# Kernel tuning notes

Hardware: AMD Instinct MI355X
Metric: run time of the kernel (lower is better)

Reference implementation:

```python
import jax, jax.numpy as jnp
import numpy as np

D_MODEL = 256      # num_nodes == d_model (forced by pre_relation mask shape)
MW = 2             # moving_window (hardcoded '2' in MPNN reshape)
STRIDE = 1
DECAY = 0.7
INPUT_DIM = 64
OUTPUT_DIM = 64
BN_EPS = 1e-5


def _mask_matrix():
    # Mask_Matrix: block (i,j) of size d_model x d_model equals decay**|i-j|
    blocks = DECAY ** np.abs(np.arange(MW)[:, None] - np.arange(MW)[None, :])
    return jnp.asarray(np.kron(blocks, np.ones((D_MODEL, D_MODEL))).astype(np.float32))


def _bn(h, w, b):
    # training-mode BatchNorm1d over channel-last layout [B, N, C]
    mu = h.mean(axis=(0, 1))
    var = h.var(axis=(0, 1))  # biased variance, as torch uses for normalization
    return (h - mu) * jax.lax.rsqrt(var + BN_EPS) * w + b


def setup_inputs() -> dict:
    key = jax.random.key(0)
    ks = jax.random.split(key, 4)
    bs, scale_num = 16, 17
    x = jax.random.normal(ks[0], (bs, scale_num, D_MODEL, INPUT_DIM), jnp.float32)
    # mapping2 weights scaled small to keep the dot-product softmax well conditioned
    w_map2 = jax.random.normal(ks[1], (INPUT_DIM, INPUT_DIM), jnp.float32) * 0.05
    b_map2 = jnp.zeros((INPUT_DIM,), jnp.float32)
    bn0_w = jnp.ones((INPUT_DIM,), jnp.float32)
    bn0_b = jnp.zeros((INPUT_DIM,), jnp.float32)
    th0_w = jax.random.normal(ks[2], (OUTPUT_DIM, INPUT_DIM), jnp.float32) / np.float32(np.sqrt(INPUT_DIM))
    th0_b = jnp.zeros((OUTPUT_DIM,), jnp.float32)
    th1_w = jax.random.normal(ks[3], (OUTPUT_DIM, INPUT_DIM), jnp.float32) / np.float32(np.sqrt(INPUT_DIM))
    th1_b = jnp.zeros((OUTPUT_DIM,), jnp.float32)
    bn1_w = jnp.ones((OUTPUT_DIM,), jnp.float32)
    bn1_b = jnp.zeros((OUTPUT_DIM,), jnp.float32)
    return dict(x=x, w_map2=w_map2, b_map2=b_map2, bn0_w=bn0_w, bn0_b=bn0_b,
                th0_w=th0_w, th0_b=th0_b, th1_w=th1_w, th1_b=th1_b,
                bn1_w=bn1_w, bn1_b=bn1_b)


def reference(x, w_map2, b_map2, bn0_w, bn0_b, th0_w, th0_b, th1_w, th1_b, bn1_w, bn1_b):
    bs, S, N, F = x.shape
    L = (S - MW) // STRIDE + 1  # num_windows from F.unfold
    # WindowConv_Graph + transpose(2,3) + reshape: X[b,l,m,n,f] = x[b, l*stride+m, n, f]
    idx = np.arange(L)[:, None] * STRIDE + np.arange(MW)[None, :]
    X = x[:, idx].reshape(bs * L, MW * N, F)  # [B', N1, F]

    # Dot_Graph_Construction_weights (N1 != d_model -> mapping2 branch)
    nf = X @ w_map2.T + b_map2                       # [B', N1, F]
    adj = jnp.einsum('bnf,bmf->bnm', nf, nf)         # [B', N1, N1]
    eye = jnp.eye(MW * N, dtype=x.dtype)
    adj = jax.nn.leaky_relu(adj - eye * 1e8)
    adj = jax.nn.softmax(adj, axis=-1) + eye

    # decay mask multiply
    adj = adj * _mask_matrix()

    # BatchNorm over input_dim channels
    xb = _bn(nf, bn0_w, bn0_b)

    # MPNN_mk_v2, field=2, way='sum'
    out = (adj @ xb) @ th0_w.T + th0_b               # hop 1
    adj2 = adj @ adj
    out = out + (adj2 @ xb) @ th1_w.T + th1_b        # hop 2
    out = jax.nn.leaky_relu(_bn(out, bn1_w, bn1_b))

    # pooling over the moving_window axis (mean), then over windows (mean)
    out = out.reshape(bs, L, MW, N, OUTPUT_DIM).mean(axis=2)
    return out.mean(axis=1)  # [bs, num_nodes, output_dim]
```

## Files before the change

### kernel.cpp

```cpp
#include <hip/hip_runtime.h>


typedef unsigned short u16;
typedef __bf16 bf16x8 __attribute__((ext_vector_type(8)));
typedef float f32x4 __attribute__((ext_vector_type(4)));
typedef unsigned int u32x4 __attribute__((ext_vector_type(4)));

#define MFMA16(a, b, c) __builtin_amdgcn_mfma_f32_16x16x32_bf16(a, b, c, 0, 0, 0)

#define BSZ 16
#define SNUM 17
#define FD 64
#define NB 256
#define N1 512
#define SL_ELEMS 16384
#define Y_ELEMS (BSZ * SNUM * SL_ELEMS)

#define WM_O 0
#define BM_O 4096
#define B0W_O 4160
#define B0B_O 4224
#define T0W_O 4288
#define T0B_O 8384
#define T1W_O 8448
#define T1B_O 12544
#define B1W_O 12608
#define B1B_O 12672
#define P_TOT 12736

#define SLAB2_O 32768
#define RED_O 65536
#define SCR_O 65792
#define LDS_U16 (SCR_O + 16 * 640)

__device__ __forceinline__ float bf2f(u16 u) {
    union { unsigned int i; float f; } v;
    v.i = ((unsigned int)u) << 16;
    return v.f;
}
__device__ __forceinline__ u16 f2bu(float f) {
    __bf16 h = (__bf16)f;
    return __builtin_bit_cast(u16, h);
}
__device__ __forceinline__ u16 f2bf(float f) {
    unsigned int u = __builtin_bit_cast(unsigned int, f);
    unsigned int r = (u + 0x7fffu + ((u >> 16) & 1u)) >> 16;
    return (u16)r;
}
__device__ __forceinline__ bf16x8 ld8g(const u16* p) {
    return __builtin_bit_cast(bf16x8, *reinterpret_cast<const u32x4*>(p));
}

__global__ __launch_bounds__(256) void k_prep(
    const void* p0, const void* p1, const void* p2, const void* p3,
    const void* p4, const void* p5, const void* p6, const void* p7,
    const void* p8, const void* p9, int* __restrict__ flagOut,
    u16* __restrict__ pc, float* __restrict__ stats) {
    const int tid = threadIdx.x, lane = tid & 63;
    int z = 0, bc = 0;
    const unsigned int* w = (const unsigned int*)p0;
    for (int i = lane; i < 2048; i += 64) {
        const unsigned int v = w[i];
        z += ((v & 0xffffu) == 0u);
        bc += (v >> 14) & 1;
    }
#pragma unroll
    for (int o = 1; o < 64; o <<= 1) {
        z += __shfl_xor(z, o);
        bc += __shfl_xor(bc, o);
    }
    const int flag = (z > 1024 || bc > 256) ? 1 : 0;
    if (blockIdx.x == 0) {
        if (tid == 0) *flagOut = flag;
        if (tid < 256) stats[tid] = 0.f;
    }
    const int i = blockIdx.x * 256 + tid;
    if (i >= P_TOT) return;
    const void* src;
    int si;
    if (i < BM_O)        { src = p0; si = i; }
    else if (i < B0W_O)  { src = p1; si = i - BM_O; }
    else if (i < B0B_O)  { src = p2; si = i - B0W_O; }
    else if (i < T0W_O)  { src = p3; si = i - B0B_O; }
    else if (i < T0B_O)  { src = p4; si = i - T0W_O; }
    else if (i < T1W_O)  { src = p5; si = i - T0B_O; }
    else if (i < T1B_O)  { src = p6; si = i - T1W_O; }
    else if (i < B1W_O)  { src = p7; si = i - T1B_O; }
    else if (i < B1B_O)  { src = p8; si = i - B1W_O; }
    else                 { src = p9; si = i - B1B_O; }
    pc[i] = flag ? f2bf(((const float*)src)[si]) : ((const u16*)src)[si];
}

__global__ __launch_bounds__(256) void k_y(const void* __restrict__ xv,
                                           const int* __restrict__ flag,
                                           const u16* __restrict__ pc,
                                           u16* __restrict__ y,
                                           float* __restrict__ gstats) {
    const int slice = blockIdx.x;
    const int tid = threadIdx.x, wave = tid >> 6, lane = tid & 63;
    const int quad = lane >> 4, l16 = lane & 15;
    __shared__ float red[128];
    if (tid < 128) red[tid] = 0.f;
    const int isf32 = *flag;

    f32x4 acc[4][4];
#pragma unroll
    for (int i = 0; i < 4; i++)
#pragma unroll
        for (int j = 0; j < 4; j++) acc[i][j] = (f32x4){0.f, 0.f, 0.f, 0.f};

    bf16x8 bfr[4][2];
#pragma unroll
    for (int nt = 0; nt < 4; nt++)
#pragma unroll
        for (int kh = 0; kh < 2; kh++)
            bfr[nt][kh] = ld8g(pc + WM_O + (nt * 16 + l16) * 64 + kh * 32 + quad * 8);

    const float* xf = (const float*)xv + (size_t)slice * SL_ELEMS;
    const u16* xh = (const u16*)xv + (size_t)slice * SL_ELEMS;

#pragma unroll
    for (int mt = 0; mt < 4; mt++) {
        const int row = wave * 64 + mt * 16 + l16;
        bf16x8 a0, a1;
        if (isf32) {
            const float* r0 = xf + row * 64 + quad * 8;
            f32x4 v0 = *(const f32x4*)r0;
            f32x4 v1 = *(const f32x4*)(r0 + 4);
            f32x4 v2 = *(const f32x4*)(r0 + 32);
            f32x4 v3 = *(const f32x4*)(r0 + 36);
#pragma unroll
            for (int j = 0; j < 4; j++) {
                a0[j] = (__bf16)v0[j]; a0[4 + j] = (__bf16)v1[j];
                a1[j] = (__bf16)v2[j]; a1[4 + j] = (__bf16)v3[j];
            }
        } else {
            a0 = ld8g(xh + row * 64 + quad * 8);
            a1 = ld8g(xh + row * 64 + 32 + quad * 8);
        }
#pragma unroll
        for (int nt = 0; nt < 4; nt++)
            acc[mt][nt] = MFMA16(a1, bfr[nt][1], MFMA16(a0, bfr[nt][0], acc[mt][nt]));
    }

    u16* ys = y + (size_t)slice * SL_ELEMS;
    float s1[4] = {0.f, 0.f, 0.f, 0.f}, s2[4] = {0.f, 0.f, 0.f, 0.f};
#pragma unroll
    for (int nt = 0; nt < 4; nt++) {
        const int col = nt * 16 + l16;
        const float bias = bf2f(pc[BM_O + col]);
#pragma unroll
        for (int mt = 0; mt < 4; mt++)
#pragma unroll
            for (int r = 0; r < 4; r++) {
                const int row = wave * 64 + mt * 16 + quad * 4 + r;
                const float v = acc[mt][nt][r] + bias;
                ys[row * 64 + col] = f2bu(v);
                s1[nt] += v;
                s2[nt] += v * v;
            }
        s1[nt] += __shfl_xor(s1[nt], 16); s1[nt] += __shfl_xor(s1[nt], 32);
        s2[nt] += __shfl_xor(s2[nt], 16); s2[nt] += __shfl_xor(s2[nt], 32);
    }
    __syncthreads();
    if (quad == 0) {
#pragma unroll
        for (int nt = 0; nt < 4; nt++) {
            atomicAdd(&red[nt * 16 + l16], s1[nt]);
            atomicAdd(&red[64 + nt * 16 + l16], s2[nt]);
        }
    }
    __syncthreads();
    const int s = slice % SNUM;
    const float wgt = (s == 0 || s == SNUM - 1) ? 1.f : 2.f;
    if (tid < 128) atomicAdd(&gstats[tid], red[tid] * wgt);
}

__global__ __launch_bounds__(1024)
__attribute__((amdgpu_waves_per_eu(4, 4)))
void k_mega(
    const u16* __restrict__ y, float* __restrict__ stats,
    const u16* __restrict__ pc, u16* __restrict__ opre) {
    __shared__ u16 lds[LDS_U16];
    u16* slab1 = lds;
    u16* slab2 = lds + SLAB2_O;
    float* red = (float*)(lds + RED_O);
    const int tid = threadIdx.x, w = tid >> 6, lane = tid & 63;
    const int quad = lane >> 4, l16 = lane & 15;
    u16* scr = lds + SCR_O + w * 640;
    const int p = blockIdx.x, b = p >> 4, l = p & 15;
    const f32x4 ZERO4 = (f32x4){0.f, 0.f, 0.f, 0.f};

    if (tid < 128) red[tid] = 0.f;

    const float cinv = 1.f / 131072.f;
    const int fme = tid & 63;
    float mu0 = stats[fme] * cinv;
    float vr0 = fmaxf(stats[64 + fme] * cinv - mu0 * mu0, 0.f);
    const float scale_f = rsqrtf(vr0 + 1e-5f) * bf2f(pc[B0W_O + fme]);
    const float shift_f = bf2f(pc[B0B_O + fme]) - mu0 * scale_f;

    const u16* ybase = y + (size_t)(b * SNUM + l) * SL_ELEMS;
#pragma unroll
    for (int i = 0; i < 4; i++) {
        const int gid = i * 1024 + tid, n = gid >> 3, g = gid & 7;
        *(u32x4*)(slab1 + n * 64 + ((g ^ (n & 7)) << 3)) =
            *(const u32x4*)(ybase + n * 64 + g * 8);
    }
    __syncthreads();

#pragma unroll
    for (int i = 0; i < 4; i++) {
        const int gn = (tid >> 6) + i * 16;
        union { u16 u[8]; u32x4 v; } pk;
#pragma unroll
        for (int j = 0; j < 8; j++) {
            const int n = gn * 8 + j;
            const u16 raw = slab1[n * 64 + (((fme >> 3) ^ (n & 7)) << 3) + (fme & 7)];
            pk.u[j] = f2bu(bf2f(raw) * scale_f + shift_f);
        }
        *(u32x4*)(slab2 + fme * 512 + ((gn ^ fme) << 3)) = pk.v;
    }
    __syncthreads();

    bf16x8 a[2][2];
#pragma unroll
    for (int st = 0; st < 2; st++)
#pragma unroll
        for (int h = 0; h < 2; h++) {
            const int row = w * 32 + st * 16 + l16;
            a[st][h] = *(const bf16x8*)(slab1 + row * 64 + (((h * 4 + quad) ^ (row & 7)) << 3));
        }

    const float mb = (w < 8) ? 0.7f : (1.0f / 0.7f);
    const float me = (w < 8) ? (1.0f / 0.7f) : 1.0f;

#pragma unroll 1
    for (int pass = 0; pass < 2; pass++) {
        f32x4 oacc[2][4];
        f32x4 lsum[2];
#pragma unroll
        for (int st = 0; st < 2; st++) {
            lsum[st] = ZERO4;
#pragma unroll
            for (int ft = 0; ft < 4; ft++) oacc[st][ft] = ZERO4;
        }

#pragma unroll 1
        for (int c = 0; c < 8; c++) {
            if (c == 4) {
#pragma unroll
                for (int st = 0; st < 2; st++)
#pragma unroll
                    for (int r = 0; r < 4; r++) lsum[st][r] *= mb;
            }
            const float lmf = ((w >= 8) == (c >= 4)) ? 0.f : -0.5145731728f;
#pragma unroll
            for (int ch = 0; ch < 2; ch++) {
                const int colbase = c * 64 + ch * 32;
                f32x4 S[2][2];
#pragma unroll
                for (int jt = 0; jt < 2; jt++) {
                    const int rj = colbase + jt * 16 + l16;
                    const bf16x8 b0 = *(const bf16x8*)(slab1 + rj * 64 + ((quad ^ (rj & 7)) << 3));
                    const bf16x8 b1 = *(const bf16x8*)(slab1 + rj * 64 + (((4 + quad) ^ (rj & 7)) << 3));
#pragma unroll
                    for (int st = 0; st < 2; st++)
                        S[st][jt] = MFMA16(a[st][1], b1, MFMA16(a[st][0], b0, ZERO4));
                }
                bf16x8 pa[2];
#pragma unroll
                for (int st = 0; st < 2; st++) {
                    const int rowbase = w * 32 + st * 16;
#pragma unroll
                    for (int jt = 0; jt < 2; jt++)
#pragma unroll
                        for (int r = 0; r < 4; r++) {
                            const float s = S[st][jt][r];
                            const float m2 = s > 0.f ? 1.44269504f : 0.0144269504f;
                            float pv = exp2f(fminf(fmaf(s, m2, lmf), 86.f));
                            if (colbase + jt * 16 == rowbase && l16 == quad * 4 + r) pv = 0.f;
                            lsum[st][r] += pv;
                            scr[(quad * 4 + r) * 40 + jt * 16 + l16] = f2bu(pv);
                        }
                    pa[st] = *(const bf16x8*)(scr + l16 * 40 + quad * 8);
                }
#pragma unroll
                for (int ft = 0; ft < 4; ft++) {
                    const int f = ft * 16 + l16, gn = c * 8 + ch * 4 + quad;
                    const bf16x8 bv = *(const bf16x8*)(slab2 + f * 512 + ((gn ^ f) << 3));
                    oacc[0][ft] = MFMA16(pa[0], bv, oacc[0][ft]);
                    oacc[1][ft] = MFMA16(pa[1], bv, oacc[1][ft]);
                }
            }
        }
#pragma unroll
        for (int st = 0; st < 2; st++)
#pragma unroll
            for (int r = 0; r < 4; r++) {
                lsum[st][r] += __shfl_xor(lsum[st][r], 1);
                lsum[st][r] += __shfl_xor(lsum[st][r], 2);
                lsum[st][r] += __shfl_xor(lsum[st][r], 4);
                lsum[st][r] += __shfl_xor(lsum[st][r], 8);
            }

        if (pass == 0) {
#pragma unroll
            for (int st = 0; st < 2; st++) {
                f32x4 inv;
#pragma unroll
                for (int r = 0; r < 4; r++) inv[r] = __builtin_amdgcn_rcpf(lsum[st][r] * me);
#pragma unroll
                for (int ft = 0; ft < 4; ft++)
#pragma unroll
                    for (int r = 0; r < 4; r++) {
                        const int i = w * 32 + st * 16 + quad * 4 + r;
                        const int f = ft * 16 + l16;
                        const float xbv = bf2f(slab2[f * 512 + (((i >> 3) ^ f) << 3) + (i & 7)]);
                        oacc[st][ft][r] = oacc[st][ft][r] * inv[r] + xbv;
                    }
            }
            __syncthreads();
#pragma unroll
            for (int st = 0; st < 2; st++)
#pragma unroll
                for (int ft = 0; ft < 4; ft++)
#pragma unroll
                    for (int r = 0; r < 4; r++) {
                        const int i = w * 32 + st * 16 + quad * 4 + r;
                        const int f = ft * 16 + l16;
                        slab2[f * 512 + (((i >> 3) ^ f) << 3) + (i & 7)] = f2bu(oacc[st][ft][r]);
                    }
            __syncthreads();
        } else {
            float s1a[4] = {0.f, 0.f, 0.f, 0.f}, s2a[4] = {0.f, 0.f, 0.f, 0.f};
#pragma unroll
            for (int st = 0; st < 2; st++) {
                f32x4 inv;
#pragma unroll
                for (int r = 0; r < 4; r++) inv[r] = __builtin_amdgcn_rcpf(lsum[st][r] * me);
#pragma unroll
                for (int ft = 0; ft < 4; ft++)
#pragma unroll
                    for (int r = 0; r < 4; r++) {
                        const int i = w * 32 + st * 16 + quad * 4 + r;
                        const int f = ft * 16 + l16;
                        const float o1 = bf2f(slab2[f * 512 + (((i >> 3) ^ f) << 3) + (i & 7)]);
                        oacc[st][ft][r] = oacc[st][ft][r] * inv[r] + o1;
                    }
                bf16x8 a1[2], a2[2];
                const int irow = w * 32 + st * 16 + l16;
#pragma unroll
                for (int h = 0; h < 2; h++)
#pragma unroll
                    for (int j = 0; j < 8; j++) {
                        const int f = h * 32 + quad * 8 + j;
                        const u16 raw = slab2[f * 512 + (((irow >> 3) ^ f) << 3) + (irow & 7)];
                        a1[h][j] = __builtin_bit_cast(__bf16, raw);
                    }
#pragma unroll
                for (int h = 0; h < 2; h++) {
#pragma unroll
                    for (int ftl = 0; ftl < 2; ftl++)
#pragma unroll
                        for (int r = 0; r < 4; r++)
                            scr[(quad * 4 + r) * 40 + ftl * 16 + l16] = f2bu(oacc[st][2 * h + ftl][r]);
                    a2[h] = *(const bf16x8*)(scr + l16 * 40 + quad * 8);
                }
                f32x4 pacc[4];
#pragma unroll
                for (int ot = 0; ot < 4; ot++) {
                    const int o = ot * 16 + l16;
                    const float bias = bf2f(pc[T0B_O + o]) + bf2f(pc[T1B_O + o]);
                    pacc[ot] = (f32x4){bias, bias, bias, bias};
                }
#pragma unroll
                for (int h = 0; h < 2; h++)
#pragma unroll
                    for (int ot = 0; ot < 4; ot++) {
                        const int o = ot * 16 + l16;
                        bf16x8 w0f = ld8g(pc + T0W_O + o * 64 + h * 32 + quad * 8);
                        bf16x8 w1f = ld8g(pc + T1W_O + o * 64 + h * 32 + quad * 8);
                        pacc[ot] = MFMA16(a1[h], w0f, pacc[ot]);
                        pacc[ot] = MFMA16(a2[h], w1f, pacc[ot]);
                    }
#pragma unroll
                for (int ot = 0; ot < 4; ot++)
#pragma unroll
                    for (int r = 0; r < 4; r++) {
                        const int i = w * 32 + st * 16 + quad * 4 + r;
                        const int o = ot * 16 + l16;
                        const float v = pacc[ot][r];
                        s1a[ot] += v;
                        s2a[ot] += v * v;
                        opre[(size_t)p * (N1 * FD) + (size_t)i * 64 + o] = f2bu(v);
                    }
            }
#pragma unroll
            for (int ot = 0; ot < 4; ot++) {
                s1a[ot] += __shfl_xor(s1a[ot], 16); s1a[ot] += __shfl_xor(s1a[ot], 32);
                s2a[ot] += __shfl_xor(s2a[ot], 16); s2a[ot] += __shfl_xor(s2a[ot], 32);
            }
            if (quad == 0) {
#pragma unroll
                for (int ot = 0; ot < 4; ot++) {
                    atomicAdd(&red[ot * 16 + l16], s1a[ot]);
                    atomicAdd(&red[64 + ot * 16 + l16], s2a[ot]);
                }
            }
            __syncthreads();
            if (tid < 128) atomicAdd(&stats[128 + tid], red[tid]);
        }
    }
}

__global__ __launch_bounds__(256) void k_final(const u16* __restrict__ op,
                                               const float* __restrict__ stats,
                                               const u16* __restrict__ pc,
                                               float* __restrict__ out) {
    const int o = blockIdx.x * 256 + threadIdx.x;
    const int f = o & 63, n = (o >> 6) & 255, b = o >> 14;
    const float inv = 1.f / 131072.f;
    const float mu = stats[128 + f] * inv;
    const float var = fmaxf(stats[192 + f] * inv - mu * mu, 0.f);
    const float rs = rsqrtf(var + 1e-5f);
    const float scale = rs * bf2f(pc[B1W_O + f]);
    const float shift = bf2f(pc[B1B_O + f]) - mu * scale;
    float acc = 0.f;
    for (int l = 0; l < 16; l++) {
        const size_t pb = (size_t)(b * 16 + l) * N1 * FD;
#pragma unroll
        for (int m = 0; m < 2; m++) {
            float v = bf2f(op[pb + (size_t)(m * 256 + n) * 64 + f]);
            v = v * scale + shift;
            acc += (v > 0.f ? v : 0.01f * v);
        }
    }
    out[o] = acc * (1.f / 32.f);
}

extern "C" void kernel_launch(void* const* d_in, const int* in_sizes, int n_in,
                              void* d_out, int out_size, void* d_ws, size_t ws_size,
                              hipStream_t stream) {
    char* ws = (char*)d_ws;
    size_t off = 0;
    auto alloc = [&](size_t bytes) { void* pp = ws + off; off += (bytes + 255) & ~(size_t)255; return pp; };
    u16* y = (u16*)alloc((size_t)Y_ELEMS * 2);
    u16* opre = (u16*)alloc((size_t)NB * N1 * FD * 2);
    u16* pc = (u16*)alloc(P_TOT * 2);
    float* stats = (float*)alloc(256 * 4);
    int* flag = (int*)alloc(256);
    float* out = (float*)d_out;

    k_prep<<<50, 256, 0, stream>>>(d_in[1], d_in[2], d_in[3], d_in[4], d_in[5],
                                   d_in[6], d_in[7], d_in[8], d_in[9], d_in[10],
                                   flag, pc, stats);
    k_y<<<BSZ * SNUM, 256, 0, stream>>>(d_in[0], flag, pc, y, stats);
    k_mega<<<NB, 1024, 0, stream>>>(y, stats, pc, opre);
    k_final<<<1024, 256, 0, stream>>>(opre, stats, pc, out);
}
```

Before: 200.8 us.

## Split mega kernel into two hop kernels over half-row blocks

```diff
diff --git a/kernel.cpp b/kernel.cpp
--- a/kernel.cpp
+++ b/kernel.cpp
@@ -31,7 +31,7 @@
 #define SLAB2_O 32768
 #define RED_O 65536
 #define SCR_O 65792
-#define LDS_U16 (SCR_O + 16 * 640)
+#define LDS_U16 (SCR_O + 8 * 640)
 
 __device__ __forceinline__ float bf2f(u16 u) {
     union { unsigned int i; float f; } v;
@@ -176,11 +176,157 @@
     if (tid < 128) atomicAdd(&gstats[tid], red[tid] * wgt);
 }
 
-__global__ __launch_bounds__(1024)
-__attribute__((amdgpu_waves_per_eu(4, 4)))
-void k_mega(
-    const u16* __restrict__ y, float* __restrict__ stats,
-    const u16* __restrict__ pc, u16* __restrict__ opre) {
+__device__ __forceinline__ void stage_slab1(u16* slab1, const u16* ybase,
+                                            int tid) {
+#pragma unroll
+    for (int i = 0; i < 8; i++) {
+        const int gid = i * 512 + tid, n = gid >> 3, g = gid & 7;
+        *(u32x4*)(slab1 + n * 64 + ((g ^ (n & 7)) << 3)) =
+            *(const u32x4*)(ybase + n * 64 + g * 8);
+    }
+}
+
+__global__ __launch_bounds__(512)
+__attribute__((amdgpu_waves_per_eu(2, 2)))
+void k_h1(const u16* __restrict__ y, const float* __restrict__ stats,
+          const u16* __restrict__ pc, u16* __restrict__ z1g) {
+    __shared__ u16 lds[LDS_U16];
+    u16* slab1 = lds;
+    u16* slab2 = lds + SLAB2_O;
+    const int tid = threadIdx.x, w = tid >> 6, lane = tid & 63;
+    const int quad = lane >> 4, l16 = lane & 15;
+    u16* scr = lds + SCR_O + w * 640;
+    const int g = blockIdx.x, p = g >> 1, half = g & 1;
+    const int b = p >> 4, l = p & 15;
+    const f32x4 ZERO4 = (f32x4){0.f, 0.f, 0.f, 0.f};
+
+    const float cinv = 1.f / 131072.f;
+    const int fme = tid & 63;
+    float mu0 = stats[fme] * cinv;
+    float vr0 = fmaxf(stats[64 + fme] * cinv - mu0 * mu0, 0.f);
+    const float scale_f = rsqrtf(vr0 + 1e-5f) * bf2f(pc[B0W_O + fme]);
+    const float shift_f = bf2f(pc[B0B_O + fme]) - mu0 * scale_f;
+
+    const u16* ybase = y + (size_t)(b * SNUM + l) * SL_ELEMS;
+    stage_slab1(slab1, ybase, tid);
+    __syncthreads();
+
+#pragma unroll
+    for (int i = 0; i < 8; i++) {
+        const int gn = w + i * 8;
+        union { u16 u[8]; u32x4 v; } pk;
+#pragma unroll
+        for (int j = 0; j < 8; j++) {
+            const int n = gn * 8 + j;
+            const u16 raw = slab1[n * 64 + (((fme >> 3) ^ (n & 7)) << 3) + (fme & 7)];
+            pk.u[j] = f2bu(bf2f(raw) * scale_f + shift_f);
+        }
+        *(u32x4*)(slab2 + fme * 512 + ((gn ^ fme) << 3)) = pk.v;
+    }
+    __syncthreads();
+
+    bf16x8 a[2][2];
+#pragma unroll
+    for (int st = 0; st < 2; st++)
+#pragma unroll
+        for (int h = 0; h < 2; h++) {
+            const int row = half * 256 + w * 32 + st * 16 + l16;
+            a[st][h] = *(const bf16x8*)(slab1 + row * 64 + (((h * 4 + quad) ^ (row & 7)) << 3));
+        }
+
+    const float mb = (half == 0) ? 0.7f : (1.0f / 0.7f);
+    const float me = (half == 0) ? (1.0f / 0.7f) : 1.0f;
+
+    f32x4 oacc[2][4];
+    f32x4 lsum[2];
+#pragma unroll
+    for (int st = 0; st < 2; st++) {
+        lsum[st] = ZERO4;
+#pragma unroll
+        for (int ft = 0; ft < 4; ft++) oacc[st][ft] = ZERO4;
+    }
+
+#pragma unroll 1
+    for (int c = 0; c < 8; c++) {
+        if (c == 4) {
+#pragma unroll
+            for (int st = 0; st < 2; st++)
+#pragma unroll
+                for (int r = 0; r < 4; r++) lsum[st][r] *= mb;
+        }
+        const float lmf = ((half == 1) == (c >= 4)) ? 0.f : -0.5145731728f;
+#pragma unroll
+        for (int ch = 0; ch < 2; ch++) {
+            const int colbase = c * 64 + ch * 32;
+            f32x4 S[2][2];
+#pragma unroll
+            for (int jt = 0; jt < 2; jt++) {
+                const int rj = colbase + jt * 16 + l16;
+                const bf16x8 b0 = *(const bf16x8*)(slab1 + rj * 64 + ((quad ^ (rj & 7)) << 3));
+                const bf16x8 b1 = *(const bf16x8*)(slab1 + rj * 64 + (((4 + quad) ^ (rj & 7)) << 3));
+#pragma unroll
+                for (int st = 0; st < 2; st++)
+                    S[st][jt] = MFMA16(a[st][1], b1, MFMA16(a[st][0], b0, ZERO4));
+            }
+            bf16x8 pa[2];
+#pragma unroll
+            for (int st = 0; st < 2; st++) {
+                const int rowbase = half * 256 + w * 32 + st * 16;
+#pragma unroll
+                for (int jt = 0; jt < 2; jt++)
+#pragma unroll
+                    for (int r = 0; r < 4; r++) {
+                        const float s = S[st][jt][r];
+                        const float m2 = s > 0.f ? 1.44269504f : 0.0144269504f;
+                        float pv = exp2f(fminf(fmaf(s, m2, lmf), 86.f));
+                        if (colbase + jt * 16 == rowbase && l16 == quad * 4 + r) pv = 0.f;
+                        lsum[st][r] += pv;
+                        scr[(quad * 4 + r) * 40 + jt * 16 + l16] = f2bu(pv);
+                    }
+                pa[st] = *(const bf16x8*)(scr + l16 * 40 + quad * 8);
+            }
+#pragma unroll
+            for (int ft = 0; ft < 4; ft++) {
+                const int f = ft * 16 + l16, gn = c * 8 + ch * 4 + quad;
+                const bf16x8 bv = *(const bf16x8*)(slab2 + f * 512 + ((gn ^ f) << 3));
+                oacc[0][ft] = MFMA16(pa[0], bv, oacc[0][ft]);
+                oacc[1][ft] = MFMA16(pa[1], bv, oacc[1][ft]);
+            }
+        }
+    }
+#pragma unroll
+    for (int st = 0; st < 2; st++)
+#pragma unroll
+        for (int r = 0; r < 4; r++) {
+            lsum[st][r] += __shfl_xor(lsum[st][r], 1);
+            lsum[st][r] += __shfl_xor(lsum[st][r], 2);
+            lsum[st][r] += __shfl_xor(lsum[st][r], 4);
+            lsum[st][r] += __shfl_xor(lsum[st][r], 8);
+        }
+
+#pragma unroll
+    for (int st = 0; st < 2; st++) {
+        f32x4 inv;
+#pragma unroll
+        for (int r = 0; r < 4; r++) inv[r] = __builtin_amdgcn_rcpf(lsum[st][r] * me);
+#pragma unroll
+        for (int ft = 0; ft < 4; ft++)
+#pragma unroll
+            for (int r = 0; r < 4; r++) {
+                const int i = half * 256 + w * 32 + st * 16 + quad * 4 + r;
+                const int f = ft * 16 + l16;
+                const float xbv = bf2f(slab2[f * 512 + (((i >> 3) ^ f) << 3) + (i & 7)]);
+                z1g[(size_t)p * (N1 * FD) + (size_t)i * 64 + f] =
+                    f2bu(oacc[st][ft][r] * inv[r] + xbv);
+            }
+    }
+}
+
+__global__ __launch_bounds__(512)
+__attribute__((amdgpu_waves_per_eu(2, 2)))
+void k_h2(const u16* __restrict__ y, const u16* __restrict__ z1g,
+          float* __restrict__ stats, const u16* __restrict__ pc,
+          u16* __restrict__ opre) {
     __shared__ u16 lds[LDS_U16];
     u16* slab1 = lds;
     u16* slab2 = lds + SLAB2_O;
@@ -188,36 +334,25 @@
     const int tid = threadIdx.x, w = tid >> 6, lane = tid & 63;
     const int quad = lane >> 4, l16 = lane & 15;
     u16* scr = lds + SCR_O + w * 640;
-    const int p = blockIdx.x, b = p >> 4, l = p & 15;
+    const int g = blockIdx.x, p = g >> 1, half = g & 1;
+    const int b = p >> 4, l = p & 15;
     const f32x4 ZERO4 = (f32x4){0.f, 0.f, 0.f, 0.f};
+    const int fme = tid & 63;
 
     if (tid < 128) red[tid] = 0.f;
 
-    const float cinv = 1.f / 131072.f;
-    const int fme = tid & 63;
-    float mu0 = stats[fme] * cinv;
-    float vr0 = fmaxf(stats[64 + fme] * cinv - mu0 * mu0, 0.f);
-    const float scale_f = rsqrtf(vr0 + 1e-5f) * bf2f(pc[B0W_O + fme]);
-    const float shift_f = bf2f(pc[B0B_O + fme]) - mu0 * scale_f;
-
     const u16* ybase = y + (size_t)(b * SNUM + l) * SL_ELEMS;
-#pragma unroll
-    for (int i = 0; i < 4; i++) {
-        const int gid = i * 1024 + tid, n = gid >> 3, g = gid & 7;
-        *(u32x4*)(slab1 + n * 64 + ((g ^ (n & 7)) << 3)) =
-            *(const u32x4*)(ybase + n * 64 + g * 8);
-    }
-    __syncthreads();
-
-#pragma unroll
-    for (int i = 0; i < 4; i++) {
-        const int gn = (tid >> 6) + i * 16;
+    stage_slab1(slab1, ybase, tid);
+
+    const u16* zbase = z1g + (size_t)p * (N1 * FD);
+#pragma unroll
+    for (int i = 0; i < 8; i++) {
+        const int gn = w + i * 8;
         union { u16 u[8]; u32x4 v; } pk;
 #pragma unroll
         for (int j = 0; j < 8; j++) {
             const int n = gn * 8 + j;
-            const u16 raw = slab1[n * 64 + (((fme >> 3) ^ (n & 7)) << 3) + (fme & 7)];
-            pk.u[j] = f2bu(bf2f(raw) * scale_f + shift_f);
+            pk.u[j] = zbase[n * 64 + fme];
         }
         *(u32x4*)(slab2 + fme * 512 + ((gn ^ fme) << 3)) = pk.v;
     }
@@ -228,190 +363,157 @@
     for (int st = 0; st < 2; st++)
 #pragma unroll
         for (int h = 0; h < 2; h++) {
-            const int row = w * 32 + st * 16 + l16;
+            const int row = half * 256 + w * 32 + st * 16 + l16;
             a[st][h] = *(const bf16x8*)(slab1 + row * 64 + (((h * 4 + quad) ^ (row & 7)) << 3));
         }
 
-    const float mb = (w < 8) ? 0.7f : (1.0f / 0.7f);
-    const float me = (w < 8) ? (1.0f / 0.7f) : 1.0f;
+    const float mb = (half == 0) ? 0.7f : (1.0f / 0.7f);
+    const float me = (half == 0) ? (1.0f / 0.7f) : 1.0f;
+
+    f32x4 oacc[2][4];
+    f32x4 lsum[2];
+#pragma unroll
+    for (int st = 0; st < 2; st++) {
+        lsum[st] = ZERO4;
+#pragma unroll
+        for (int ft = 0; ft < 4; ft++) oacc[st][ft] = ZERO4;
+    }
 
 #pragma unroll 1
-    for (int pass = 0; pass < 2; pass++) {
-        f32x4 oacc[2][4];
-        f32x4 lsum[2];
-#pragma unroll
-        for (int st = 0; st < 2; st++) {
-            lsum[st] = ZERO4;
-#pragma unroll
-            for (int ft = 0; ft < 4; ft++) oacc[st][ft] = ZERO4;
-        }
-
-#pragma unroll 1
-        for (int c = 0; c < 8; c++) {
-            if (c == 4) {
+    for (int c = 0; c < 8; c++) {
+        if (c == 4) {
+#pragma unroll
+            for (int st = 0; st < 2; st++)
+#pragma unroll
+                for (int r = 0; r < 4; r++) lsum[st][r] *= mb;
+        }
+        const float lmf = ((half == 1) == (c >= 4)) ? 0.f : -0.5145731728f;
+#pragma unroll
+        for (int ch = 0; ch < 2; ch++) {
+            const int colbase = c * 64 + ch * 32;
+            f32x4 S[2][2];
+#pragma unroll
+            for (int jt = 0; jt < 2; jt++) {
+                const int rj = colbase + jt * 16 + l16;
+                const bf16x8 b0 = *(const bf16x8*)(slab1 + rj * 64 + ((quad ^ (rj & 7)) << 3));
+                const bf16x8 b1 = *(const bf16x8*)(slab1 + rj * 64 + (((4 + quad) ^ (rj & 7)) << 3));
 #pragma unroll
                 for (int st = 0; st < 2; st++)
-#pragma unroll
-                    for (int r = 0; r < 4; r++) lsum[st][r] *= mb;
-            }
-            const float lmf = ((w >= 8) == (c >= 4)) ? 0.f : -0.5145731728f;
-#pragma unroll
-            for (int ch = 0; ch < 2; ch++) {
-                const int colbase = c * 64 + ch * 32;
-                f32x4 S[2][2];
-#pragma unroll
-                for (int jt = 0; jt < 2; jt++) {
-                    const int rj = colbase + jt * 16 + l16;
-                    const bf16x8 b0 = *(const bf16x8*)(slab1 + rj * 64 + ((quad ^ (rj & 7)) << 3));
-                    const bf16x8 b1 = *(const bf16x8*)(slab1 + rj * 64 + (((4 + quad) ^ (rj & 7)) << 3));
-#pragma unroll
-                    for (int st = 0; st < 2; st++)
-                        S[st][jt] = MFMA16(a[st][1], b1, MFMA16(a[st][0], b0, ZERO4));
-                }
-                bf16x8 pa[2];
-#pragma unroll
-                for (int st = 0; st < 2; st++) {
-                    const int rowbase = w * 32 + st * 16;
-#pragma unroll
-                    for (int jt = 0; jt < 2; jt++)
-#pragma unroll
-                        for (int r = 0; r < 4; r++) {
-                            const float s = S[st][jt][r];
-                            const float m2 = s > 0.f ? 1.44269504f : 0.0144269504f;
-                            float pv = exp2f(fminf(fmaf(s, m2, lmf), 86.f));
-                            if (colbase + jt * 16 == rowbase && l16 == quad * 4 + r) pv = 0.f;
-                            lsum[st][r] += pv;
-                            scr[(quad * 4 + r) * 40 + jt * 16 + l16] = f2bu(pv);
-                        }
-                    pa[st] = *(const bf16x8*)(scr + l16 * 40 + quad * 8);
-                }
-#pragma unroll
-                for (int ft = 0; ft < 4; ft++) {
-                    const int f = ft * 16 + l16, gn = c * 8 + ch * 4 + quad;
-                    const bf16x8 bv = *(const bf16x8*)(slab2 + f * 512 + ((gn ^ f) << 3));
-                    oacc[0][ft] = MFMA16(pa[0], bv, oacc[0][ft]);
-                    oacc[1][ft] = MFMA16(pa[1], bv, oacc[1][ft]);
-                }
-            }
-        }
-#pragma unroll
-        for (int st = 0; st < 2; st++)
+                    S[st][jt] = MFMA16(a[st][1], b1, MFMA16(a[st][0], b0, ZERO4));
+            }
+            bf16x8 pa[2];
+#pragma unroll
+            for (int st = 0; st < 2; st++) {
+                const int rowbase = half * 256 + w * 32 + st * 16;
+#pragma unroll
+                for (int jt = 0; jt < 2; jt++)
+#pragma unroll
+                    for (int r = 0; r < 4; r++) {
+                        const float s = S[st][jt][r];
+                        const float m2 = s > 0.f ? 1.44269504f : 0.0144269504f;
+                        float pv = exp2f(fminf(fmaf(s, m2, lmf), 86.f));
+                        if (colbase + jt * 16 == rowbase && l16 == quad * 4 + r) pv = 0.f;
+                        lsum[st][r] += pv;
+                        scr[(quad * 4 + r) * 40 + jt * 16 + l16] = f2bu(pv);
+                    }
+                pa[st] = *(const bf16x8*)(scr + l16 * 40 + quad * 8);
+            }
+#pragma unroll
+            for (int ft = 0; ft < 4; ft++) {
+                const int f = ft * 16 + l16, gn = c * 8 + ch * 4 + quad;
+                const bf16x8 bv = *(const bf16x8*)(slab2 + f * 512 + ((gn ^ f) << 3));
+                oacc[0][ft] = MFMA16(pa[0], bv, oacc[0][ft]);
+                oacc[1][ft] = MFMA16(pa[1], bv, oacc[1][ft]);
+            }
+        }
+    }
+#pragma unroll
+    for (int st = 0; st < 2; st++)
+#pragma unroll
+        for (int r = 0; r < 4; r++) {
+            lsum[st][r] += __shfl_xor(lsum[st][r], 1);
+            lsum[st][r] += __shfl_xor(lsum[st][r], 2);
+            lsum[st][r] += __shfl_xor(lsum[st][r], 4);
+            lsum[st][r] += __shfl_xor(lsum[st][r], 8);
+        }
+
+    float s1a[4] = {0.f, 0.f, 0.f, 0.f}, s2a[4] = {0.f, 0.f, 0.f, 0.f};
+#pragma unroll
+    for (int st = 0; st < 2; st++) {
+        f32x4 inv;
+#pragma unroll
+        for (int r = 0; r < 4; r++) inv[r] = __builtin_amdgcn_rcpf(lsum[st][r] * me);
+#pragma unroll
+        for (int ft = 0; ft < 4; ft++)
 #pragma unroll
             for (int r = 0; r < 4; r++) {
-                lsum[st][r] += __shfl_xor(lsum[st][r], 1);
-                lsum[st][r] += __shfl_xor(lsum[st][r], 2);
-                lsum[st][r] += __shfl_xor(lsum[st][r], 4);
-                lsum[st][r] += __shfl_xor(lsum[st][r], 8);
-            }
-
-        if (pass == 0) {
-#pragma unroll
-            for (int st = 0; st < 2; st++) {
-                f32x4 inv;
-#pragma unroll
-                for (int r = 0; r < 4; r++) inv[r] = __builtin_amdgcn_rcpf(lsum[st][r] * me);
-#pragma unroll
-                for (int ft = 0; ft < 4; ft++)
-#pragma unroll
-                    for (int r = 0; r < 4; r++) {
-                        const int i = w * 32 + st * 16 + quad * 4 + r;
-                        const int f = ft * 16 + l16;
-                        const float xbv = bf2f(slab2[f * 512 + (((i >> 3) ^ f) << 3) + (i & 7)]);
-                        oacc[st][ft][r] = oacc[st][ft][r] * inv[r] + xbv;
-                    }
-            }
-            __syncthreads();
-#pragma unroll
-            for (int st = 0; st < 2; st++)
-#pragma unroll
-                for (int ft = 0; ft < 4; ft++)
-#pragma unroll
-                    for (int r = 0; r < 4; r++) {
-                        const int i = w * 32 + st * 16 + quad * 4 + r;
-                        const int f = ft * 16 + l16;
-                        slab2[f * 512 + (((i >> 3) ^ f) << 3) + (i & 7)] = f2bu(oacc[st][ft][r]);
-                    }
-            __syncthreads();
-        } else {
-            float s1a[4] = {0.f, 0.f, 0.f, 0.f}, s2a[4] = {0.f, 0.f, 0.f, 0.f};
-#pragma unroll
-            for (int st = 0; st < 2; st++) {
-                f32x4 inv;
-#pragma unroll
-                for (int r = 0; r < 4; r++) inv[r] = __builtin_amdgcn_rcpf(lsum[st][r] * me);
-#pragma unroll
-                for (int ft = 0; ft < 4; ft++)
-#pragma unroll
-                    for (int r = 0; r < 4; r++) {
-                        const int i = w * 32 + st * 16 + quad * 4 + r;
-                        const int f = ft * 16 + l16;
-                        const float o1 = bf2f(slab2[f * 512 + (((i >> 3) ^ f) << 3) + (i & 7)]);
-                        oacc[st][ft][r] = oacc[st][ft][r] * inv[r] + o1;
-                    }
-                bf16x8 a1[2], a2[2];
-                const int irow = w * 32 + st * 16 + l16;
-#pragma unroll
-                for (int h = 0; h < 2; h++)
-#pragma unroll
-                    for (int j = 0; j < 8; j++) {
-                        const int f = h * 32 + quad * 8 + j;
-                        const u16 raw = slab2[f * 512 + (((irow >> 3) ^ f) << 3) + (irow & 7)];
-                        a1[h][j] = __builtin_bit_cast(__bf16, raw);
-                    }
-#pragma unroll
-                for (int h = 0; h < 2; h++) {
-#pragma unroll
-                    for (int ftl = 0; ftl < 2; ftl++)
-#pragma unroll
-                        for (int r = 0; r < 4; r++)
-                            scr[(quad * 4 + r) * 40 + ftl * 16 + l16] = f2bu(oacc[st][2 * h + ftl][r]);
-                    a2[h] = *(const bf16x8*)(scr + l16 * 40 + quad * 8);
-                }
-                f32x4 pacc[4];
-#pragma unroll
-                for (int ot = 0; ot < 4; ot++) {
-                    const int o = ot * 16 + l16;
-                    const float bias = bf2f(pc[T0B_O + o]) + bf2f(pc[T1B_O + o]);
-                    pacc[ot] = (f32x4){bias, bias, bias, bias};
-                }
-#pragma unroll
-                for (int h = 0; h < 2; h++)
-#pragma unroll
-                    for (int ot = 0; ot < 4; ot++) {
-                        const int o = ot * 16 + l16;
-                        bf16x8 w0f = ld8g(pc + T0W_O + o * 64 + h * 32 + quad * 8);
-                        bf16x8 w1f = ld8g(pc + T1W_O + o * 64 + h * 32 + quad * 8);
-                        pacc[ot] = MFMA16(a1[h], w0f, pacc[ot]);
-                        pacc[ot] = MFMA16(a2[h], w1f, pacc[ot]);
-                    }
-#pragma unroll
-                for (int ot = 0; ot < 4; ot++)
-#pragma unroll
-                    for (int r = 0; r < 4; r++) {
-                        const int i = w * 32 + st * 16 + quad * 4 + r;
-                        const int o = ot * 16 + l16;
-                        const float v = pacc[ot][r];
-                        s1a[ot] += v;
-                        s2a[ot] += v * v;
-                        opre[(size_t)p * (N1 * FD) + (size_t)i * 64 + o] = f2bu(v);
-                    }
-            }
+                const int i = half * 256 + w * 32 + st * 16 + quad * 4 + r;
+                const int f = ft * 16 + l16;
+                const float o1 = bf2f(slab2[f * 512 + (((i >> 3) ^ f) << 3) + (i & 7)]);
+                oacc[st][ft][r] = oacc[st][ft][r] * inv[r] + o1;
+            }
+        bf16x8 a1[2], a2[2];
+        const int irow = half * 256 + w * 32 + st * 16 + l16;
+#pragma unroll
+        for (int h = 0; h < 2; h++)
+#pragma unroll
+            for (int j = 0; j < 8; j++) {
+                const int f = h * 32 + quad * 8 + j;
+                const u16 raw = slab2[f * 512 + (((irow >> 3) ^ f) << 3) + (irow & 7)];
+                a1[h][j] = __builtin_bit_cast(__bf16, raw);
+            }
+#pragma unroll
+        for (int h = 0; h < 2; h++) {
+#pragma unroll
+            for (int ftl = 0; ftl < 2; ftl++)
+#pragma unroll
+                for (int r = 0; r < 4; r++)
+                    scr[(quad * 4 + r) * 40 + ftl * 16 + l16] = f2bu(oacc[st][2 * h + ftl][r]);
+            a2[h] = *(const bf16x8*)(scr + l16 * 40 + quad * 8);
+        }
+        f32x4 pacc[4];
+#pragma unroll
+        for (int ot = 0; ot < 4; ot++) {
+            const int o = ot * 16 + l16;
+            const float bias = bf2f(pc[T0B_O + o]) + bf2f(pc[T1B_O + o]);
+            pacc[ot] = (f32x4){bias, bias, bias, bias};
+        }
+#pragma unroll
+        for (int h = 0; h < 2; h++)
 #pragma unroll
             for (int ot = 0; ot < 4; ot++) {
-                s1a[ot] += __shfl_xor(s1a[ot], 16); s1a[ot] += __shfl_xor(s1a[ot], 32);
-                s2a[ot] += __shfl_xor(s2a[ot], 16); s2a[ot] += __shfl_xor(s2a[ot], 32);
-            }
-            if (quad == 0) {
-#pragma unroll
-                for (int ot = 0; ot < 4; ot++) {
-                    atomicAdd(&red[ot * 16 + l16], s1a[ot]);
-                    atomicAdd(&red[64 + ot * 16 + l16], s2a[ot]);
-                }
-            }
-            __syncthreads();
-            if (tid < 128) atomicAdd(&stats[128 + tid], red[tid]);
-        }
-    }
+                const int o = ot * 16 + l16;
+                bf16x8 w0f = ld8g(pc + T0W_O + o * 64 + h * 32 + quad * 8);
+                bf16x8 w1f = ld8g(pc + T1W_O + o * 64 + h * 32 + quad * 8);
+                pacc[ot] = MFMA16(a1[h], w0f, pacc[ot]);
+                pacc[ot] = MFMA16(a2[h], w1f, pacc[ot]);
+            }
+#pragma unroll
+        for (int ot = 0; ot < 4; ot++)
+#pragma unroll
+            for (int r = 0; r < 4; r++) {
+                const int i = half * 256 + w * 32 + st * 16 + quad * 4 + r;
+                const int o = ot * 16 + l16;
+                const float v = pacc[ot][r];
+                s1a[ot] += v;
+                s2a[ot] += v * v;
+                opre[(size_t)p * (N1 * FD) + (size_t)i * 64 + o] = f2bu(v);
+            }
+    }
+#pragma unroll
+    for (int ot = 0; ot < 4; ot++) {
+        s1a[ot] += __shfl_xor(s1a[ot], 16); s1a[ot] += __shfl_xor(s1a[ot], 32);
+        s2a[ot] += __shfl_xor(s2a[ot], 16); s2a[ot] += __shfl_xor(s2a[ot], 32);
+    }
+    if (quad == 0) {
+#pragma unroll
+        for (int ot = 0; ot < 4; ot++) {
+            atomicAdd(&red[ot * 16 + l16], s1a[ot]);
+            atomicAdd(&red[64 + ot * 16 + l16], s2a[ot]);
+        }
+    }
+    __syncthreads();
+    if (tid < 128) atomicAdd(&stats[128 + tid], red[tid]);
 }
 
 __global__ __launch_bounds__(256) void k_final(const u16* __restrict__ op,
@@ -446,6 +548,7 @@
     size_t off = 0;
     auto alloc = [&](size_t bytes) { void* pp = ws + off; off += (bytes + 255) & ~(size_t)255; return pp; };
     u16* y = (u16*)alloc((size_t)Y_ELEMS * 2);
+    u16* z1 = (u16*)alloc((size_t)NB * N1 * FD * 2);
     u16* opre = (u16*)alloc((size_t)NB * N1 * FD * 2);
     u16* pc = (u16*)alloc(P_TOT * 2);
     float* stats = (float*)alloc(256 * 4);
@@ -456,6 +559,7 @@
                                    d_in[6], d_in[7], d_in[8], d_in[9], d_in[10],
                                    flag, pc, stats);
     k_y<<<BSZ * SNUM, 256, 0, stream>>>(d_in[0], flag, pc, y, stats);
-    k_mega<<<NB, 1024, 0, stream>>>(y, stats, pc, opre);
+    k_h1<<<2 * NB, 512, 0, stream>>>(y, stats, pc, z1);
+    k_h2<<<2 * NB, 512, 0, stream>>>(y, z1, stats, pc, opre);
     k_final<<<1024, 256, 0, stream>>>(opre, stats, pc, out);
 }
```

After: 213.7 us. 6.4% more time.
